# Optimization experiments

Measured on AMD Instinct MI355X. Metric: run time of the kernel, lower is better.

## Reference

```python
import jax, jax.numpy as jnp
import numpy as np

N_NODES = 100000
N_EDGES = 640000
D_IN = 128
D_OUT = 128

def setup_inputs() -> dict:
    key = jax.random.key(0)
    k1, k2, k3, k4, k5 = jax.random.split(key, 5)
    feat = jax.random.normal(k1, (N_NODES, D_IN), dtype=jnp.float32)
    src = jax.random.randint(k2, (N_EDGES,), 0, N_NODES, dtype=jnp.int32)
    dst = jax.random.randint(k3, (N_EDGES,), 0, N_NODES, dtype=jnp.int32)
    scale = 1.0 / np.sqrt(D_IN)
    W_self = jax.random.normal(k4, (D_IN, D_OUT), dtype=jnp.float32) * scale
    W_neigh = jax.random.normal(k5, (D_IN, D_OUT), dtype=jnp.float32) * scale
    b_self = jnp.zeros((D_OUT,), dtype=jnp.float32)
    b_neigh = jnp.zeros((D_OUT,), dtype=jnp.float32)
    return {"feat": feat, "src": src, "dst": dst,
            "W_self": W_self, "b_self": b_self,
            "W_neigh": W_neigh, "b_neigh": b_neigh}

def reference(feat, src, dst, W_self, b_self, W_neigh, b_neigh):
    # GraphSAGE 'mean' aggregator: copy_src + mean reduce over in-edges, then
    # rst = fc_self(h_self) + fc_neigh(h_neigh). feat_drop=0, no activation/norm.
    n = feat.shape[0]
    msg = feat[src]                                   # [E, D_in] gather
    neigh_sum = jax.ops.segment_sum(msg, dst, num_segments=n)      # [N, D_in]
    deg = jax.ops.segment_sum(jnp.ones_like(dst, dtype=feat.dtype), dst,
                              num_segments=n)          # [N]
    # mean with zero-in-degree nodes -> 0 (DGL semantics)
    h_neigh = neigh_sum / jnp.maximum(deg, 1.0)[:, None]
    rst = feat @ W_self + b_self + h_neigh @ W_neigh + b_neigh      # [N, D_out]
    return rst
```

## Files before the change

### kernel.cpp

```cpp
#include <hip/hip_runtime.h>


constexpr int N_NODES = 100000;
constexpr int N_EDGES = 640000;
constexpr int D = 128;

constexpr int SCAN_NBLOCKS = 98;

constexpr int NXCD = 8;
constexpr int XRANGE = (N_NODES + NXCD - 1) / NXCD;
constexpr int FILL_BPG = 250;
constexpr int FILL_EPB = N_EDGES / FILL_BPG;

typedef __attribute__((ext_vector_type(8))) short bf16x8;
typedef __attribute__((ext_vector_type(4))) float f32x4;

__device__ __forceinline__ unsigned short f2bf(float f) {
    unsigned int u = __float_as_uint(f);
    unsigned int r = u + 0x7FFFu + ((u >> 16) & 1u);
    return (unsigned short)(r >> 16);
}
__device__ __forceinline__ float bflo(unsigned int v) { return __uint_as_float(v << 16); }
__device__ __forceinline__ float bfhi(unsigned int v) { return __uint_as_float(v & 0xFFFF0000u); }

__global__ __launch_bounds__(256) void zero_deg_kernel(int4* __restrict__ deg4) {
    int i = blockIdx.x * 256 + threadIdx.x;
    if (i < N_NODES / 4) deg4[i] = int4{0, 0, 0, 0};
}

__global__ void prepass_kernel(const int* __restrict__ dst, int* __restrict__ deg,
                               const float* __restrict__ Ws, const float* __restrict__ Wn,
                               unsigned short* __restrict__ wp,
                               const float* __restrict__ feat, unsigned short* __restrict__ fb,
                               int* __restrict__ ctr) {
    const int gid = blockIdx.x * blockDim.x + threadIdx.x;
    if (gid == 0) ctr[0] = 0;
    if (gid < N_EDGES) atomicAdd(&deg[dst[gid]], 1);
    if (gid < 2 * D * D) {
        int i = gid;
        int r  = i & 7;
        int c  = (i >> 3) & 127;
        int h  = (i >> 10) & 3;
        int ks = (i >> 12) & 3;
        int m  = i >> 14;
        const float* W = m ? Wn : Ws;
        int k = ks * 32 + h * 8 + r;
        wp[i] = f2bf(W[k * D + c]);
    }
    const int total4 = N_NODES * D / 4;
    for (int i = gid; i < total4; i += N_EDGES) {
        float4 v = ((const float4*)feat)[i];
        ushort4 o;
        o.x = f2bf(v.x); o.y = f2bf(v.y); o.z = f2bf(v.z); o.w = f2bf(v.w);
        ((ushort4*)fb)[i] = o;
    }
}

__global__ __launch_bounds__(256) void scan_kernel(const int* __restrict__ deg,
                                                   int* __restrict__ rowptr,
                                                   int* __restrict__ cursor,
                                                   int* __restrict__ bsum,
                                                   int* __restrict__ ctr) {
    __shared__ int wsum[4];
    const int tid = threadIdx.x;
    const int lane = tid & 63;
    const int wave = tid >> 6;
    const int base = (blockIdx.x * 256 + tid) * 4;

    int local[4];
    int tsum = 0;
    #pragma unroll
    for (int j = 0; j < 4; j++) {
        int idx = base + j;
        local[j] = (idx < N_NODES) ? deg[idx] : 0;
        tsum += local[j];
    }
    {
        int s = tsum;
        for (int off = 32; off > 0; off >>= 1) s += __shfl_down(s, off, 64);
        if (lane == 0) wsum[wave] = s;
        __syncthreads();
        if (tid == 0) bsum[blockIdx.x] = wsum[0] + wsum[1] + wsum[2] + wsum[3];
    }
    __syncthreads();
    if (tid == 0) {
        __threadfence();
        __hip_atomic_fetch_add(ctr, 1, __ATOMIC_ACQ_REL, __HIP_MEMORY_SCOPE_AGENT);
        while (__hip_atomic_load(ctr, __ATOMIC_ACQUIRE, __HIP_MEMORY_SCOPE_AGENT)
               < SCAN_NBLOCKS) {}
    }
    __syncthreads();

    int v = (tid < blockIdx.x) ? bsum[tid] : 0;
    for (int off = 32; off > 0; off >>= 1) v += __shfl_down(v, off, 64);
    if (lane == 0) wsum[wave] = v;
    __syncthreads();
    const int boff = wsum[0] + wsum[1] + wsum[2] + wsum[3];
    __syncthreads();

    int incl = tsum;
    for (int off = 1; off < 64; off <<= 1) {
        int u = __shfl_up(incl, off, 64);
        if (lane >= off) incl += u;
    }
    if (lane == 63) wsum[wave] = incl;
    __syncthreads();
    int woff = 0;
    for (int w = 0; w < 4; w++) woff += (w < wave) ? wsum[w] : 0;

    int run = boff + woff + (incl - tsum);
    #pragma unroll
    for (int j = 0; j < 4; j++) {
        int idx = base + j;
        if (idx < N_NODES) {
            rowptr[idx] = run;
            cursor[idx] = run;
            run += local[j];
        }
    }
    if (blockIdx.x == 0 && tid == 0) rowptr[N_NODES] = N_EDGES;
}

__global__ __launch_bounds__(256) void fill_kernel(const int* __restrict__ src,
                                                   const int* __restrict__ dst,
                                                   int* __restrict__ cursor,
                                                   int* __restrict__ csr_src) {
    const int xcd = blockIdx.x & (NXCD - 1);
    const int j   = blockIdx.x >> 3;
    const int lo  = xcd * XRANGE;
    const int hi  = lo + XRANGE;
    const int ebase = j * FILL_EPB;

    for (int e = ebase + threadIdx.x; e < ebase + FILL_EPB; e += 256) {
        const int d = dst[e];
        const int s = src[e];
        if (d >= lo && d < hi) {
            int pos = atomicAdd(&cursor[d], 1);
            csr_src[pos] = s;
        }
    }
}

__global__ __launch_bounds__(256) void gather_kernel(
    const unsigned short* __restrict__ fb, const int* __restrict__ csr_src,
    const int* __restrict__ rowptr, unsigned short* __restrict__ hn)
{
    const int tid = threadIdx.x;
    const int lane = tid & 63;
    const int g = lane >> 4;
    const int gl = lane & 15;
    const int wid = (blockIdx.x * blockDim.x + tid) >> 6;
    const int n = wid * 4 + g;
    if (n >= N_NODES) return;

    const int e0 = rowptr[n];
    const int e1 = rowptr[n + 1];

    float acc[8] = {0.f, 0.f, 0.f, 0.f, 0.f, 0.f, 0.f, 0.f};
    for (int base = e0; base < e1; base += 8) {
        int sidx[8];
        #pragma unroll
        for (int j = 0; j < 8; j++) {
            int ee = base + j;
            ee = (ee < e1) ? ee : (e1 - 1);
            sidx[j] = csr_src[ee];
        }
        uint4 v[8];
        #pragma unroll
        for (int j = 0; j < 8; j++)
            v[j] = ((const uint4*)(fb + (size_t)sidx[j] * D))[gl];
        #pragma unroll
        for (int j = 0; j < 8; j++) {
            const float w = (base + j < e1) ? 1.0f : 0.0f;
            acc[0] = fmaf(w, bflo(v[j].x), acc[0]);
            acc[1] = fmaf(w, bfhi(v[j].x), acc[1]);
            acc[2] = fmaf(w, bflo(v[j].y), acc[2]);
            acc[3] = fmaf(w, bfhi(v[j].y), acc[3]);
            acc[4] = fmaf(w, bflo(v[j].z), acc[4]);
            acc[5] = fmaf(w, bfhi(v[j].z), acc[5]);
            acc[6] = fmaf(w, bflo(v[j].w), acc[6]);
            acc[7] = fmaf(w, bfhi(v[j].w), acc[7]);
        }
    }
    const float sc = 1.0f / (float)max(e1 - e0, 1);
    uint4 o;
    o.x = ((unsigned int)f2bf(acc[1] * sc) << 16) | (unsigned int)f2bf(acc[0] * sc);
    o.y = ((unsigned int)f2bf(acc[3] * sc) << 16) | (unsigned int)f2bf(acc[2] * sc);
    o.z = ((unsigned int)f2bf(acc[5] * sc) << 16) | (unsigned int)f2bf(acc[4] * sc);
    o.w = ((unsigned int)f2bf(acc[7] * sc) << 16) | (unsigned int)f2bf(acc[6] * sc);
    ((uint4*)(hn + (size_t)n * D))[gl] = o;
}

__global__ __launch_bounds__(256) void mmfused_kernel(
    const unsigned short* __restrict__ fb, const unsigned short* __restrict__ hn,
    const unsigned short* __restrict__ wp,
    const float* __restrict__ b_self, const float* __restrict__ b_neigh,
    float* __restrict__ out)
{
    const int tid = threadIdx.x;
    const int wave = tid >> 6, lane = tid & 63;
    const int h = lane >> 4, c = lane & 15;
    const int row_base = blockIdx.x * 128 + wave * 32;

    bf16x8 a[2][2][4];
    #pragma unroll
    for (int ti = 0; ti < 2; ti++) {
        int row = row_base + ti * 16 + c;
        int rowc = min(row, N_NODES - 1);
        const bf16x8* f0 = (const bf16x8*)(fb + (size_t)rowc * D);
        const bf16x8* f1 = (const bf16x8*)(hn + (size_t)rowc * D);
        #pragma unroll
        for (int ks = 0; ks < 4; ks++) {
            a[0][ti][ks] = f0[ks * 4 + h];
            a[1][ti][ks] = f1[ks * 4 + h];
        }
    }

    const bf16x8* wpv = (const bf16x8*)wp;
    for (int ct = 0; ct < 8; ct++) {
        f32x4 acc[2];
        #pragma unroll
        for (int ti = 0; ti < 2; ti++) acc[ti] = f32x4{0.f, 0.f, 0.f, 0.f};

        #pragma unroll
        for (int m = 0; m < 2; m++) {
            bf16x8 b[4];
            #pragma unroll
            for (int ks = 0; ks < 4; ks++)
                b[ks] = wpv[((m * 4 + ks) * 4 + h) * 128 + ct * 16 + c];
            #pragma unroll
            for (int ks = 0; ks < 4; ks++)
                #pragma unroll
                for (int ti = 0; ti < 2; ti++)
                    acc[ti] = __builtin_amdgcn_mfma_f32_16x16x32_bf16(a[m][ti][ks], b[ks], acc[ti], 0, 0, 0);
        }

        const int col = ct * 16 + c;
        const float bias = b_self[col] + b_neigh[col];
        #pragma unroll
        for (int ti = 0; ti < 2; ti++) {
            if (row_base + ti * 16 < N_NODES) {
                #pragma unroll
                for (int q = 0; q < 4; q++) {
                    int row = row_base + ti * 16 + h * 4 + q;
                    __builtin_nontemporal_store(acc[ti][q] + bias,
                                                &out[(size_t)row * D + col]);
                }
            }
        }
    }
}

extern "C" void kernel_launch(void* const* d_in, const int* in_sizes, int n_in,
                              void* d_out, int out_size, void* d_ws, size_t ws_size,
                              hipStream_t stream) {
    const float* feat    = (const float*)d_in[0];
    const int*   src     = (const int*)d_in[1];
    const int*   dst     = (const int*)d_in[2];
    const float* W_self  = (const float*)d_in[3];
    const float* b_self  = (const float*)d_in[4];
    const float* W_neigh = (const float*)d_in[5];
    const float* b_neigh = (const float*)d_in[6];
    float* out = (float*)d_out;

    unsigned short* fb = (unsigned short*)d_ws;
    unsigned short* hn = fb + (size_t)N_NODES * D;
    unsigned short* wp = hn + (size_t)N_NODES * D;
    int*   deg     = (int*)(wp + 2 * D * D);
    int*   rowptr  = deg + N_NODES;
    int*   cursor  = rowptr + (N_NODES + 1);
    int*   csr_src = cursor + N_NODES;
    int*   bsum    = csr_src + N_EDGES;
    int*   ctr     = bsum + SCAN_NBLOCKS;

    zero_deg_kernel<<<(N_NODES / 4 + 255) / 256, 256, 0, stream>>>((int4*)deg);

    prepass_kernel<<<(N_EDGES + 255) / 256, 256, 0, stream>>>(dst, deg, W_self, W_neigh,
                                                              wp, feat, fb, ctr);

    scan_kernel<<<SCAN_NBLOCKS, 256, 0, stream>>>(deg, rowptr, cursor, bsum, ctr);

    fill_kernel<<<NXCD * FILL_BPG, 256, 0, stream>>>(src, dst, cursor, csr_src);

    gather_kernel<<<N_NODES / 16, 256, 0, stream>>>(fb, csr_src, rowptr, hn);

    mmfused_kernel<<<(N_NODES + 127) / 128, 256, 0, stream>>>(fb, hn, wp, b_self, b_neigh, out);
}
```

Measured before the change: 128.3 us.

## Fuse neighbor gather into matmul kernel and move weight packing to zero kernel

Merges the mean-aggregation gather and the dual bf16 MFMA matmul into a single kernel. Each block gathers its own 128 rows into hn, synchronises, then reads them back for the matmul, which removes one launch and lets the hn reads likely hit in cache. Weight packing moves into the zeroing kernel, and the feat-to-bf16 conversion now uses nontemporal loads. In exchange the gather phase runs with fewer waves (782 blocks, each wave handling 8 node groups serially), which may reduce the memory-level parallelism available to the random gathers.

New measurement: 135.4 us. +5.6%, slower.

```diff
diff --git a/kernel.cpp b/kernel.cpp
--- a/kernel.cpp
+++ b/kernel.cpp
@@ -23,20 +23,15 @@
 __device__ __forceinline__ float bflo(unsigned int v) { return __uint_as_float(v << 16); }
 __device__ __forceinline__ float bfhi(unsigned int v) { return __uint_as_float(v & 0xFFFF0000u); }
 
-__global__ __launch_bounds__(256) void zero_deg_kernel(int4* __restrict__ deg4) {
-    int i = blockIdx.x * 256 + threadIdx.x;
-    if (i < N_NODES / 4) deg4[i] = int4{0, 0, 0, 0};
-}
-
-__global__ void prepass_kernel(const int* __restrict__ dst, int* __restrict__ deg,
-                               const float* __restrict__ Ws, const float* __restrict__ Wn,
-                               unsigned short* __restrict__ wp,
-                               const float* __restrict__ feat, unsigned short* __restrict__ fb,
-                               int* __restrict__ ctr) {
-    const int gid = blockIdx.x * blockDim.x + threadIdx.x;
+__global__ __launch_bounds__(256) void zero_kernel(int4* __restrict__ deg4,
+                                                   int* __restrict__ ctr,
+                                                   const float* __restrict__ Ws,
+                                                   const float* __restrict__ Wn,
+                                                   unsigned short* __restrict__ wp) {
+    const int gid = blockIdx.x * 256 + threadIdx.x;
+    if (gid < N_NODES / 4) deg4[gid] = int4{0, 0, 0, 0};
     if (gid == 0) ctr[0] = 0;
-    if (gid < N_EDGES) atomicAdd(&deg[dst[gid]], 1);
-    if (gid < 2 * D * D) {
+    {
         int i = gid;
         int r  = i & 7;
         int c  = (i >> 3) & 127;
@@ -47,9 +42,17 @@
         int k = ks * 32 + h * 8 + r;
         wp[i] = f2bf(W[k * D + c]);
     }
+}
+
+__global__ void prepass_kernel(const int* __restrict__ dst, int* __restrict__ deg,
+                               const float* __restrict__ feat,
+                               unsigned short* __restrict__ fb) {
+    const int gid = blockIdx.x * blockDim.x + threadIdx.x;
+    if (gid < N_EDGES) atomicAdd(&deg[dst[gid]], 1);
     const int total4 = N_NODES * D / 4;
+    const f32x4* fv = (const f32x4*)feat;
     for (int i = gid; i < total4; i += N_EDGES) {
-        float4 v = ((const float4*)feat)[i];
+        f32x4 v = __builtin_nontemporal_load(&fv[i]);
         ushort4 o;
         o.x = f2bf(v.x); o.y = f2bf(v.y); o.z = f2bf(v.z); o.w = f2bf(v.w);
         ((ushort4*)fb)[i] = o;
@@ -141,71 +144,67 @@
     }
 }
 
-__global__ __launch_bounds__(256) void gather_kernel(
+__global__ __launch_bounds__(256) void gathermm_kernel(
     const unsigned short* __restrict__ fb, const int* __restrict__ csr_src,
-    const int* __restrict__ rowptr, unsigned short* __restrict__ hn)
-{
-    const int tid = threadIdx.x;
-    const int lane = tid & 63;
-    const int g = lane >> 4;
-    const int gl = lane & 15;
-    const int wid = (blockIdx.x * blockDim.x + tid) >> 6;
-    const int n = wid * 4 + g;
-    if (n >= N_NODES) return;
-
-    const int e0 = rowptr[n];
-    const int e1 = rowptr[n + 1];
-
-    float acc[8] = {0.f, 0.f, 0.f, 0.f, 0.f, 0.f, 0.f, 0.f};
-    for (int base = e0; base < e1; base += 8) {
-        int sidx[8];
-        #pragma unroll
-        for (int j = 0; j < 8; j++) {
-            int ee = base + j;
-            ee = (ee < e1) ? ee : (e1 - 1);
-            sidx[j] = csr_src[ee];
-        }
-        uint4 v[8];
-        #pragma unroll
-        for (int j = 0; j < 8; j++)
-            v[j] = ((const uint4*)(fb + (size_t)sidx[j] * D))[gl];
-        #pragma unroll
-        for (int j = 0; j < 8; j++) {
-            const float w = (base + j < e1) ? 1.0f : 0.0f;
-            acc[0] = fmaf(w, bflo(v[j].x), acc[0]);
-            acc[1] = fmaf(w, bfhi(v[j].x), acc[1]);
-            acc[2] = fmaf(w, bflo(v[j].y), acc[2]);
-            acc[3] = fmaf(w, bfhi(v[j].y), acc[3]);
-            acc[4] = fmaf(w, bflo(v[j].z), acc[4]);
-            acc[5] = fmaf(w, bfhi(v[j].z), acc[5]);
-            acc[6] = fmaf(w, bflo(v[j].w), acc[6]);
-            acc[7] = fmaf(w, bfhi(v[j].w), acc[7]);
-        }
-    }
-    const float sc = 1.0f / (float)max(e1 - e0, 1);
-    uint4 o;
-    o.x = ((unsigned int)f2bf(acc[1] * sc) << 16) | (unsigned int)f2bf(acc[0] * sc);
-    o.y = ((unsigned int)f2bf(acc[3] * sc) << 16) | (unsigned int)f2bf(acc[2] * sc);
-    o.z = ((unsigned int)f2bf(acc[5] * sc) << 16) | (unsigned int)f2bf(acc[4] * sc);
-    o.w = ((unsigned int)f2bf(acc[7] * sc) << 16) | (unsigned int)f2bf(acc[6] * sc);
-    ((uint4*)(hn + (size_t)n * D))[gl] = o;
-}
-
-__global__ __launch_bounds__(256) void mmfused_kernel(
-    const unsigned short* __restrict__ fb, const unsigned short* __restrict__ hn,
-    const unsigned short* __restrict__ wp,
+    const int* __restrict__ rowptr, const unsigned short* __restrict__ wp,
     const float* __restrict__ b_self, const float* __restrict__ b_neigh,
-    float* __restrict__ out)
+    unsigned short* __restrict__ hn, float* __restrict__ out)
 {
     const int tid = threadIdx.x;
     const int wave = tid >> 6, lane = tid & 63;
+    const int g = lane >> 4;
+    const int gl = lane & 15;
+    const int row_base = blockIdx.x * 128;
+
+    for (int it = 0; it < 8; it++) {
+        const int n = row_base + wave * 32 + it * 4 + g;
+        if (n < N_NODES) {
+            const int e0 = rowptr[n];
+            const int e1 = rowptr[n + 1];
+            float acc[8] = {0.f, 0.f, 0.f, 0.f, 0.f, 0.f, 0.f, 0.f};
+            for (int base = e0; base < e1; base += 8) {
+                int sidx[8];
+                #pragma unroll
+                for (int j = 0; j < 8; j++) {
+                    int ee = base + j;
+                    ee = (ee < e1) ? ee : (e1 - 1);
+                    sidx[j] = csr_src[ee];
+                }
+                uint4 v[8];
+                #pragma unroll
+                for (int j = 0; j < 8; j++)
+                    v[j] = ((const uint4*)(fb + (size_t)sidx[j] * D))[gl];
+                #pragma unroll
+                for (int j = 0; j < 8; j++) {
+                    const float w = (base + j < e1) ? 1.0f : 0.0f;
+                    acc[0] = fmaf(w, bflo(v[j].x), acc[0]);
+                    acc[1] = fmaf(w, bfhi(v[j].x), acc[1]);
+                    acc[2] = fmaf(w, bflo(v[j].y), acc[2]);
+                    acc[3] = fmaf(w, bfhi(v[j].y), acc[3]);
+                    acc[4] = fmaf(w, bflo(v[j].z), acc[4]);
+                    acc[5] = fmaf(w, bfhi(v[j].z), acc[5]);
+                    acc[6] = fmaf(w, bflo(v[j].w), acc[6]);
+                    acc[7] = fmaf(w, bfhi(v[j].w), acc[7]);
+                }
+            }
+            const float sc = 1.0f / (float)max(e1 - e0, 1);
+            uint4 o;
+            o.x = ((unsigned int)f2bf(acc[1] * sc) << 16) | (unsigned int)f2bf(acc[0] * sc);
+            o.y = ((unsigned int)f2bf(acc[3] * sc) << 16) | (unsigned int)f2bf(acc[2] * sc);
+            o.z = ((unsigned int)f2bf(acc[5] * sc) << 16) | (unsigned int)f2bf(acc[4] * sc);
+            o.w = ((unsigned int)f2bf(acc[7] * sc) << 16) | (unsigned int)f2bf(acc[6] * sc);
+            ((uint4*)(hn + (size_t)n * D))[gl] = o;
+        }
+    }
+    __syncthreads();
+
     const int h = lane >> 4, c = lane & 15;
-    const int row_base = blockIdx.x * 128 + wave * 32;
+    const int wrow_base = row_base + wave * 32;
 
     bf16x8 a[2][2][4];
     #pragma unroll
     for (int ti = 0; ti < 2; ti++) {
-        int row = row_base + ti * 16 + c;
+        int row = wrow_base + ti * 16 + c;
         int rowc = min(row, N_NODES - 1);
         const bf16x8* f0 = (const bf16x8*)(fb + (size_t)rowc * D);
         const bf16x8* f1 = (const bf16x8*)(hn + (size_t)rowc * D);
@@ -239,10 +238,10 @@
         const float bias = b_self[col] + b_neigh[col];
         #pragma unroll
         for (int ti = 0; ti < 2; ti++) {
-            if (row_base + ti * 16 < N_NODES) {
+            if (wrow_base + ti * 16 < N_NODES) {
                 #pragma unroll
                 for (int q = 0; q < 4; q++) {
-                    int row = row_base + ti * 16 + h * 4 + q;
+                    int row = wrow_base + ti * 16 + h * 4 + q;
                     __builtin_nontemporal_store(acc[ti][q] + bias,
                                                 &out[(size_t)row * D + col]);
                 }
@@ -273,16 +272,14 @@
     int*   bsum    = csr_src + N_EDGES;
     int*   ctr     = bsum + SCAN_NBLOCKS;
 
-    zero_deg_kernel<<<(N_NODES / 4 + 255) / 256, 256, 0, stream>>>((int4*)deg);
-
-    prepass_kernel<<<(N_EDGES + 255) / 256, 256, 0, stream>>>(dst, deg, W_self, W_neigh,
-                                                              wp, feat, fb, ctr);
+    zero_kernel<<<128, 256, 0, stream>>>((int4*)deg, ctr, W_self, W_neigh, wp);
+
+    prepass_kernel<<<(N_EDGES + 255) / 256, 256, 0, stream>>>(dst, deg, feat, fb);
 
     scan_kernel<<<SCAN_NBLOCKS, 256, 0, stream>>>(deg, rowptr, cursor, bsum, ctr);
 
     fill_kernel<<<NXCD * FILL_BPG, 256, 0, stream>>>(src, dst, cursor, csr_src);
 
-    gather_kernel<<<N_NODES / 16, 256, 0, stream>>>(fb, csr_src, rowptr, hn);
-
-    mmfused_kernel<<<(N_NODES + 127) / 128, 256, 0, stream>>>(fb, hn, wp, b_self, b_neigh, out);
-}
+    gathermm_kernel<<<(N_NODES + 127) / 128, 256, 0, stream>>>(fb, csr_src, rowptr, wp,
+                                                               b_self, b_neigh, hn, out);
+}
```
